# Performance work log

Measured on AMD Instinct MI355X. Metric: run time of the kernel, lower is better.

The kernel has to match this reference:

```python
import jax, jax.numpy as jnp
import numpy as np

ALPHA = 0.2  # LeakyReLU negative slope
NEG_INF = -9e15


def setup_inputs() -> dict:
    key = jax.random.key(0)
    k1, k2, k3, k4 = jax.random.split(key, 4)
    B, N, F_in, F_out = 8, 2048, 512, 256
    h = jax.random.normal(k1, (B, N, F_in), dtype=jnp.float32)
    adj = jax.random.randint(k2, (B, N, N), 0, 2, dtype=jnp.int32)
    W = jax.random.normal(k3, (F_in, F_out), dtype=jnp.float32) * (1.414 / np.sqrt(F_in))
    a = jax.random.normal(k4, (2 * F_out, 1), dtype=jnp.float32) * (1.414 / np.sqrt(2 * F_out))
    return {"h": h, "adj": adj, "W": W, "a": a}


def reference(h, adj, W, a):
    # Wh: [B, N, F_out]
    Wh = jnp.matmul(h, W)
    F_out = W.shape[1]
    a1 = a[:F_out, 0]   # [F_out] -> source (row i) part
    a2 = a[F_out:, 0]   # [F_out] -> target (col j) part
    # e[b,i,j] = leakyrelu(Wh[b,i]@a1 + Wh[b,j]@a2)  (decomposed concat-attention)
    f1 = jnp.einsum('bnf,f->bn', Wh, a1)  # [B, N]
    f2 = jnp.einsum('bnf,f->bn', Wh, a2)  # [B, N]
    e = f1[:, :, None] + f2[:, None, :]   # [B, N, N]
    e = jnp.where(e > 0, e, ALPHA * e)    # LeakyReLU
    e = jnp.where(adj > 0, e, NEG_INF)
    attention = jax.nn.softmax(e, axis=2)
    # dropout p=0.0 / eval mode: identity
    h_prime = jnp.matmul(attention, Wh)   # [B, N, F_out]
    return jax.nn.elu(h_prime)            # concat=True branch
```

## Files before the change

kernel.cpp:

```cpp
#include <hip/hip_runtime.h>
#include <hip/hip_bf16.h>

#define GAT_ALPHA 0.2f

typedef short bf16x8 __attribute__((ext_vector_type(8)));
typedef float f32x4 __attribute__((ext_vector_type(4)));

__device__ __forceinline__ unsigned f2bf_u(float x) {
  union { float f; unsigned u; } v; v.f = x;
  return (v.u + 0x7fffu + ((v.u >> 16) & 1u)) >> 16;
}
__device__ __forceinline__ unsigned short f2bf(float x) { return (unsigned short)f2bf_u(x); }

__global__ void k_wt(const float* __restrict__ W, unsigned short* __restrict__ WT) {
  int kb = blockIdx.x * 8;
  int f = threadIdx.x;
  bf16x8 o;
#pragma unroll
  for (int i = 0; i < 8; ++i) o[i] = (short)f2bf(W[(kb + i) * 256 + f]);
  *reinterpret_cast<bf16x8*>(WT + f * 512 + kb) = o;
}

__global__ __launch_bounds__(256, 2) void k_gemm1(
    const float* __restrict__ h, const unsigned short* __restrict__ WT,
    const float* __restrict__ avec,
    unsigned short* __restrict__ WhT,
    float* __restrict__ E1p, float* __restrict__ E1n,
    float* __restrict__ E2p, float* __restrict__ E2n)
{
  const int bx = blockIdx.x;
  const int b = bx & 7, ng = bx >> 3;
  const int n0 = ng * 32;
  const int t = threadIdx.x;
  const int lane = t & 63, w = t >> 6;
  const int l15 = lane & 15, q = lane >> 4;

  __shared__ __align__(16) unsigned short Wt[256 * 36];
  __shared__ float f1a[32], f2a[32];
  if (t < 32) { f1a[t] = 0.f; f2a[t] = 0.f; }

  f32x4 acc[4][2];
#pragma unroll
  for (int i = 0; i < 4; ++i)
#pragma unroll
    for (int j = 0; j < 2; ++j) acc[i][j] = (f32x4){0.f, 0.f, 0.f, 0.f};

  const size_t hbase = ((size_t)(b * 2048 + n0)) * 512;
  const unsigned short* wtb = WT + (w * 64 + l15) * 512 + q * 8;
  const float* hrow0 = h + hbase + (size_t)l15 * 512 + q * 8;
  const float* hrow1 = h + hbase + (size_t)(16 + l15) * 512 + q * 8;

  bf16x8 afA[4], afN[4];
  float4 hA[4], hB[4], hN[4];
#pragma unroll
  for (int mt = 0; mt < 4; ++mt) afA[mt] = *reinterpret_cast<const bf16x8*>(wtb + mt * 16 * 512);
  hA[0] = *reinterpret_cast<const float4*>(hrow0);
  hA[1] = *reinterpret_cast<const float4*>(hrow0 + 4);
  hA[2] = *reinterpret_cast<const float4*>(hrow1);
  hA[3] = *reinterpret_cast<const float4*>(hrow1 + 4);
  hB[0] = *reinterpret_cast<const float4*>(hrow0 + 32);
  hB[1] = *reinterpret_cast<const float4*>(hrow0 + 36);
  hB[2] = *reinterpret_cast<const float4*>(hrow1 + 32);
  hB[3] = *reinterpret_cast<const float4*>(hrow1 + 36);

#pragma unroll
  for (int k = 0; k < 16; ++k) {
    if (k < 15) {
      const unsigned short* p = wtb + (k + 1) * 32;
#pragma unroll
      for (int mt = 0; mt < 4; ++mt) afN[mt] = *reinterpret_cast<const bf16x8*>(p + mt * 16 * 512);
    }
    if (k < 14) {
      int o = (k + 2) * 32;
      hN[0] = *reinterpret_cast<const float4*>(hrow0 + o);
      hN[1] = *reinterpret_cast<const float4*>(hrow0 + o + 4);
      hN[2] = *reinterpret_cast<const float4*>(hrow1 + o);
      hN[3] = *reinterpret_cast<const float4*>(hrow1 + o + 4);
    }
    bf16x8 bfr[2];
#pragma unroll
    for (int nt = 0; nt < 2; ++nt) {
      float4 x0 = hA[nt * 2], x1 = hA[nt * 2 + 1];
      bf16x8 bb;
      bb[0] = (short)f2bf(x0.x); bb[1] = (short)f2bf(x0.y);
      bb[2] = (short)f2bf(x0.z); bb[3] = (short)f2bf(x0.w);
      bb[4] = (short)f2bf(x1.x); bb[5] = (short)f2bf(x1.y);
      bb[6] = (short)f2bf(x1.z); bb[7] = (short)f2bf(x1.w);
      bfr[nt] = bb;
    }
#pragma unroll
    for (int mt = 0; mt < 4; ++mt)
#pragma unroll
      for (int nt = 0; nt < 2; ++nt)
        acc[mt][nt] = __builtin_amdgcn_mfma_f32_16x16x32_bf16(afA[mt], bfr[nt], acc[mt][nt], 0, 0, 0);
    if (k < 15) {
#pragma unroll
      for (int mt = 0; mt < 4; ++mt) afA[mt] = afN[mt];
#pragma unroll
      for (int i = 0; i < 4; ++i) hA[i] = hB[i];
#pragma unroll
      for (int i = 0; i < 4; ++i) hB[i] = hN[i];
    }
  }

  float s1[2] = {0.f, 0.f}, s2[2] = {0.f, 0.f};
#pragma unroll
  for (int mt = 0; mt < 4; ++mt) {
#pragma unroll
    for (int nt = 0; nt < 2; ++nt) {
#pragma unroll
      for (int r = 0; r < 4; ++r) {
        int f = w * 64 + mt * 16 + q * 4 + r;
        float v = acc[mt][nt][r];
        Wt[f * 36 + nt * 16 + l15] = f2bf(v);
        s1[nt] += v * avec[f];
        s2[nt] += v * avec[256 + f];
      }
    }
  }
#pragma unroll
  for (int nt = 0; nt < 2; ++nt) {
    s1[nt] += __shfl_xor(s1[nt], 16); s1[nt] += __shfl_xor(s1[nt], 32);
    s2[nt] += __shfl_xor(s2[nt], 16); s2[nt] += __shfl_xor(s2[nt], 32);
  }
  __syncthreads();
  if (q == 0) {
#pragma unroll
    for (int nt = 0; nt < 2; ++nt) {
      atomicAdd(&f1a[nt * 16 + l15], s1[nt]);
      atomicAdd(&f2a[nt * 16 + l15], s2[nt]);
    }
  }
#pragma unroll
  for (int i = 0; i < 8; ++i) {
    int f = i * 32 + (t >> 3), g = t & 7;
    uint2 v = *reinterpret_cast<const uint2*>(Wt + f * 36 + g * 4);
    *reinterpret_cast<uint2*>(WhT + (size_t)(b * 256 + f) * 2048 + n0 + g * 4) = v;
  }
  __syncthreads();
  if (t < 32) {
    int n = b * 2048 + n0 + t;
    float f1 = f1a[t], f2 = f2a[t];
    E1p[n] = __expf(f1);
    E1n[n] = __expf(GAT_ALPHA * f1);
    E2p[n] = __expf(f2);
    E2n[n] = __expf(GAT_ALPHA * f2);
  }
}

__device__ __forceinline__ void build_frag(
    unsigned short* dst, int4 alo, int4 ahi, float e1p, float e1n,
    float4 epl, float4 eph, float4 enl, float4 enh, float& den)
{
  float p0 = alo.x ? fmaxf(e1p * epl.x, e1n * enl.x) : 0.f;
  float p1 = alo.y ? fmaxf(e1p * epl.y, e1n * enl.y) : 0.f;
  float p2 = alo.z ? fmaxf(e1p * epl.z, e1n * enl.z) : 0.f;
  float p3 = alo.w ? fmaxf(e1p * epl.w, e1n * enl.w) : 0.f;
  float p4 = ahi.x ? fmaxf(e1p * eph.x, e1n * enh.x) : 0.f;
  float p5 = ahi.y ? fmaxf(e1p * eph.y, e1n * enh.y) : 0.f;
  float p6 = ahi.z ? fmaxf(e1p * eph.z, e1n * enh.z) : 0.f;
  float p7 = ahi.w ? fmaxf(e1p * eph.w, e1n * enh.w) : 0.f;
  den += ((p0 + p1) + (p2 + p3)) + ((p4 + p5) + (p6 + p7));
  uint4 pk;
  pk.x = f2bf_u(p0) | (f2bf_u(p1) << 16);
  pk.y = f2bf_u(p2) | (f2bf_u(p3) << 16);
  pk.z = f2bf_u(p4) | (f2bf_u(p5) << 16);
  pk.w = f2bf_u(p6) | (f2bf_u(p7) << 16);
  *reinterpret_cast<uint4*>(dst) = pk;
}

__global__ __launch_bounds__(512, 2) void k_gat(
    const int* __restrict__ adj, const unsigned short* __restrict__ WhT,
    const float* __restrict__ E1p, const float* __restrict__ E1n,
    const float* __restrict__ E2p, const float* __restrict__ E2n,
    float* __restrict__ out)
{
  const int bx = blockIdx.x;
  const int b = bx & 7, ig = bx >> 3;
  const int i0 = ig * 64;
  const int t = threadIdx.x;
  const int lane = t & 63, w = t >> 6;
  const int l15 = lane & 15, q = lane >> 4;
  const int m = t & 15, qk = (t >> 4) & 3, pp = t >> 6;
  const int rt0 = pp >> 2, ks = pp & 3;
  const int r0 = rt0 * 16 + m, r1 = r0 + 32;
  const int cb = ks * 32 + qk * 8;

  __shared__ __align__(16) unsigned short Pb[2][8192];
  __shared__ float den_l[64];
  if (t < 64) den_l[t] = 0.f;

  const float e1p0 = E1p[b * 2048 + i0 + r0], e1n0 = E1n[b * 2048 + i0 + r0];
  const float e1p1 = E1p[b * 2048 + i0 + r1], e1n1 = E1n[b * 2048 + i0 + r1];
  float d0 = 0.f, d1 = 0.f;

  f32x4 acc[4][2];
#pragma unroll
  for (int i = 0; i < 4; ++i)
#pragma unroll
    for (int j = 0; j < 2; ++j) acc[i][j] = (f32x4){0.f, 0.f, 0.f, 0.f};

  const size_t adj0 = ((size_t)(b * 2048 + i0 + r0)) * 2048 + cb;
  const size_t adj1 = adj0 + (size_t)32 * 2048;
  const int e2b = b * 2048 + cb;
  const unsigned short* Wb = WhT + (size_t)(b * 256 + w * 32) * 2048;

  int4 z0l = *reinterpret_cast<const int4*>(adj + adj0);
  int4 z0h = *reinterpret_cast<const int4*>(adj + adj0 + 4);
  int4 z1l = *reinterpret_cast<const int4*>(adj + adj1);
  int4 z1h = *reinterpret_cast<const int4*>(adj + adj1 + 4);
  float4 zpl = *reinterpret_cast<const float4*>(E2p + e2b);
  float4 zph = *reinterpret_cast<const float4*>(E2p + e2b + 4);
  float4 znl = *reinterpret_cast<const float4*>(E2n + e2b);
  float4 znh = *reinterpret_cast<const float4*>(E2n + e2b + 4);
  bf16x8 bcur[2][4], bnxt[2][4];
#pragma unroll
  for (int ct = 0; ct < 2; ++ct)
#pragma unroll
    for (int k2 = 0; k2 < 4; ++k2)
      bcur[ct][k2] = *reinterpret_cast<const bf16x8*>(
          Wb + (size_t)(ct * 16 + l15) * 2048 + k2 * 32 + q * 8);
  int4 A0l = *reinterpret_cast<const int4*>(adj + adj0 + 128);
  int4 A0h = *reinterpret_cast<const int4*>(adj + adj0 + 132);
  int4 A1l = *reinterpret_cast<const int4*>(adj + adj1 + 128);
  int4 A1h = *reinterpret_cast<const int4*>(adj + adj1 + 132);
  float4 Epl = *reinterpret_cast<const float4*>(E2p + e2b + 128);
  float4 Eph = *reinterpret_cast<const float4*>(E2p + e2b + 132);
  float4 Enl = *reinterpret_cast<const float4*>(E2n + e2b + 128);
  float4 Enh = *reinterpret_cast<const float4*>(E2n + e2b + 132);
  build_frag(&Pb[0][(pp * 64 + lane) * 8], z0l, z0h, e1p0, e1n0, zpl, zph, znl, znh, d0);
  build_frag(&Pb[0][((pp + 8) * 64 + lane) * 8], z1l, z1h, e1p1, e1n1, zpl, zph, znl, znh, d1);
  __syncthreads();

#pragma unroll
  for (int c = 0; c < 16; ++c) {
    if (c < 15) {
      const unsigned short* p = Wb + (c + 1) * 128 + q * 8;
#pragma unroll
      for (int ct = 0; ct < 2; ++ct)
#pragma unroll
        for (int k2 = 0; k2 < 4; ++k2)
          bnxt[ct][k2] = *reinterpret_cast<const bf16x8*>(p + (size_t)(ct * 16 + l15) * 2048 + k2 * 32);
    }
    int4 nA0l, nA0h, nA1l, nA1h;
    float4 nEpl, nEph, nEnl, nEnh;
    if (c < 14) {
      int o = (c + 2) * 128;
      nA0l = *reinterpret_cast<const int4*>(adj + adj0 + o);
      nA0h = *reinterpret_cast<const int4*>(adj + adj0 + o + 4);
      nA1l = *reinterpret_cast<const int4*>(adj + adj1 + o);
      nA1h = *reinterpret_cast<const int4*>(adj + adj1 + o + 4);
      nEpl = *reinterpret_cast<const float4*>(E2p + e2b + o);
      nEph = *reinterpret_cast<const float4*>(E2p + e2b + o + 4);
      nEnl = *reinterpret_cast<const float4*>(E2n + e2b + o);
      nEnh = *reinterpret_cast<const float4*>(E2n + e2b + o + 4);
    }
    const unsigned short* pb = &Pb[c & 1][0];
#pragma unroll
    for (int k2 = 0; k2 < 4; ++k2) {
      bf16x8 afr[4];
#pragma unroll
      for (int rt = 0; rt < 4; ++rt)
        afr[rt] = *reinterpret_cast<const bf16x8*>(pb + ((rt * 4 + k2) * 64 + lane) * 8);
#pragma unroll
      for (int rt = 0; rt < 4; ++rt)
#pragma unroll
        for (int ct = 0; ct < 2; ++ct)
          acc[rt][ct] = __builtin_amdgcn_mfma_f32_16x16x32_bf16(afr[rt], bcur[ct][k2], acc[rt][ct], 0, 0, 0);
    }
    if (c < 15) {
      unsigned short* wb = &Pb[(c + 1) & 1][0];
      build_frag(wb + (pp * 64 + lane) * 8, A0l, A0h, e1p0, e1n0, Epl, Eph, Enl, Enh, d0);
      build_frag(wb + ((pp + 8) * 64 + lane) * 8, A1l, A1h, e1p1, e1n1, Epl, Eph, Enl, Enh, d1);
    }
    if (c < 15) __syncthreads();
    if (c < 15) {
#pragma unroll
      for (int ct = 0; ct < 2; ++ct)
#pragma unroll
        for (int k2 = 0; k2 < 4; ++k2) bcur[ct][k2] = bnxt[ct][k2];
    }
    if (c < 14) {
      A0l = nA0l; A0h = nA0h; A1l = nA1l; A1h = nA1h;
      Epl = nEpl; Eph = nEph; Enl = nEnl; Enh = nEnh;
    }
  }

  d0 += __shfl_xor(d0, 16); d0 += __shfl_xor(d0, 32);
  d1 += __shfl_xor(d1, 16); d1 += __shfl_xor(d1, 32);
  if (lane < 16) {
    atomicAdd(&den_l[r0], d0);
    atomicAdd(&den_l[r1], d1);
  }
  __syncthreads();

#pragma unroll
  for (int rt = 0; rt < 4; ++rt) {
#pragma unroll
    for (int r = 0; r < 4; ++r) {
      int row = rt * 16 + q * 4 + r;
      float dinv = 1.0f / den_l[row];
      size_t ob = ((size_t)(b * 2048 + i0 + row)) * 256 + w * 32;
#pragma unroll
      for (int ct = 0; ct < 2; ++ct) {
        float v = acc[rt][ct][r] * dinv;
        v = v > 0.f ? v : (__expf(v) - 1.f);
        out[ob + ct * 16 + l15] = v;
      }
    }
  }
}

extern "C" void kernel_launch(void* const* d_in, const int* in_sizes, int n_in,
                              void* d_out, int out_size, void* d_ws, size_t ws_size,
                              hipStream_t stream) {
  const float* h   = (const float*)d_in[0];
  const int*   adj = (const int*)d_in[1];
  const float* W   = (const float*)d_in[2];
  const float* a   = (const float*)d_in[3];
  float* out = (float*)d_out;

  char* ws = (char*)d_ws;
  unsigned short* WhT = (unsigned short*)ws;
  unsigned short* WT  = (unsigned short*)(ws + 8388608);
  float* E1p  = (float*)(ws + 8388608 + 262144);
  float* E1n  = E1p + 16384;
  float* E2p  = E1n + 16384;
  float* E2n  = E2p + 16384;

  k_wt<<<dim3(64), dim3(256), 0, stream>>>(W, WT);
  k_gemm1<<<dim3(512), dim3(256), 0, stream>>>(h, WT, a, WhT, E1p, E1n, E2p, E2n);
  k_gat<<<dim3(256), dim3(512), 0, stream>>>(adj, WhT, E1p, E1n, E2p, E2n, out);
}
```

Before: 262.3 us.

## Pack adjacency into bitmask, shrink gemm1 tile, simplify GAT pipelining

Adds a pre-pass kernel that packs the int32 adjacency into one bit per entry, in a layout matching the GAT fragment builder. The attention kernel then reads bytes instead of int4 vectors. k_gemm1 moves to 16-row tiles with a three-deep h prefetch and occupancy hint 4, and k_gat drops the register double-buffering of WhT and adj for in-loop loads with occupancy hint 4. The pack kernel still reads the full adjacency once and adds a launch, so the main gain must come from lighter register pressure and more occupancy, while lost prefetching may expose latency.

```diff
diff --git a/kernel.cpp b/kernel.cpp
--- a/kernel.cpp
+++ b/kernel.cpp
@@ -21,7 +21,26 @@
   *reinterpret_cast<bf16x8*>(WT + f * 512 + kb) = o;
 }
 
-__global__ __launch_bounds__(256, 2) void k_gemm1(
+__global__ __launch_bounds__(256) void k_pack(const int* __restrict__ adj,
+                                              unsigned char* __restrict__ bm) {
+  __shared__ unsigned char sb[2048];
+  const int bId = blockIdx.x, t = threadIdx.x;
+  const int4* base = reinterpret_cast<const int4*>(adj + (size_t)bId * 8 * 2048);
+#pragma unroll
+  for (int i = 0; i < 8; ++i) {
+    int4 v0 = base[i * 512 + t * 2];
+    int4 v1 = base[i * 512 + t * 2 + 1];
+    unsigned by = (v0.x != 0)        | ((v0.y != 0) << 1) | ((v0.z != 0) << 2) |
+                  ((v0.w != 0) << 3) | ((v1.x != 0) << 4) | ((v1.y != 0) << 5) |
+                  ((v1.z != 0) << 6) | ((v1.w != 0) << 7);
+    sb[i * 256 + (t & 15) * 16 + (t >> 4)] = (unsigned char)by;
+  }
+  __syncthreads();
+  reinterpret_cast<uint2*>(bm + (size_t)bId * 2048)[t] =
+      reinterpret_cast<const uint2*>(sb)[t];
+}
+
+__global__ __launch_bounds__(256, 4) void k_gemm1(
     const float* __restrict__ h, const unsigned short* __restrict__ WT,
     const float* __restrict__ avec,
     unsigned short* __restrict__ WhT,
@@ -30,115 +49,85 @@
 {
   const int bx = blockIdx.x;
   const int b = bx & 7, ng = bx >> 3;
-  const int n0 = ng * 32;
+  const int n0 = ng * 16;
   const int t = threadIdx.x;
   const int lane = t & 63, w = t >> 6;
   const int l15 = lane & 15, q = lane >> 4;
 
-  __shared__ __align__(16) unsigned short Wt[256 * 36];
-  __shared__ float f1a[32], f2a[32];
-  if (t < 32) { f1a[t] = 0.f; f2a[t] = 0.f; }
-
-  f32x4 acc[4][2];
-#pragma unroll
-  for (int i = 0; i < 4; ++i)
-#pragma unroll
-    for (int j = 0; j < 2; ++j) acc[i][j] = (f32x4){0.f, 0.f, 0.f, 0.f};
-
-  const size_t hbase = ((size_t)(b * 2048 + n0)) * 512;
+  __shared__ __align__(16) unsigned short Wt[256 * 24];
+  __shared__ float f1a[16], f2a[16];
+  if (t < 16) { f1a[t] = 0.f; f2a[t] = 0.f; }
+
+  f32x4 acc[4];
+#pragma unroll
+  for (int i = 0; i < 4; ++i) acc[i] = (f32x4){0.f, 0.f, 0.f, 0.f};
+
   const unsigned short* wtb = WT + (w * 64 + l15) * 512 + q * 8;
-  const float* hrow0 = h + hbase + (size_t)l15 * 512 + q * 8;
-  const float* hrow1 = h + hbase + (size_t)(16 + l15) * 512 + q * 8;
-
-  bf16x8 afA[4], afN[4];
-  float4 hA[4], hB[4], hN[4];
-#pragma unroll
-  for (int mt = 0; mt < 4; ++mt) afA[mt] = *reinterpret_cast<const bf16x8*>(wtb + mt * 16 * 512);
-  hA[0] = *reinterpret_cast<const float4*>(hrow0);
-  hA[1] = *reinterpret_cast<const float4*>(hrow0 + 4);
-  hA[2] = *reinterpret_cast<const float4*>(hrow1);
-  hA[3] = *reinterpret_cast<const float4*>(hrow1 + 4);
-  hB[0] = *reinterpret_cast<const float4*>(hrow0 + 32);
-  hB[1] = *reinterpret_cast<const float4*>(hrow0 + 36);
-  hB[2] = *reinterpret_cast<const float4*>(hrow1 + 32);
-  hB[3] = *reinterpret_cast<const float4*>(hrow1 + 36);
+  const float* hrow = h + ((size_t)(b * 2048 + n0 + l15)) * 512 + q * 8;
+
+  float4 hS0[2], hS1[2], hS2[2];
+  hS0[0] = *reinterpret_cast<const float4*>(hrow);
+  hS0[1] = *reinterpret_cast<const float4*>(hrow + 4);
+  hS1[0] = *reinterpret_cast<const float4*>(hrow + 32);
+  hS1[1] = *reinterpret_cast<const float4*>(hrow + 36);
+  hS2[0] = *reinterpret_cast<const float4*>(hrow + 64);
+  hS2[1] = *reinterpret_cast<const float4*>(hrow + 68);
 
 #pragma unroll
   for (int k = 0; k < 16; ++k) {
-    if (k < 15) {
-      const unsigned short* p = wtb + (k + 1) * 32;
-#pragma unroll
-      for (int mt = 0; mt < 4; ++mt) afN[mt] = *reinterpret_cast<const bf16x8*>(p + mt * 16 * 512);
-    }
-    if (k < 14) {
-      int o = (k + 2) * 32;
-      hN[0] = *reinterpret_cast<const float4*>(hrow0 + o);
-      hN[1] = *reinterpret_cast<const float4*>(hrow0 + o + 4);
-      hN[2] = *reinterpret_cast<const float4*>(hrow1 + o);
-      hN[3] = *reinterpret_cast<const float4*>(hrow1 + o + 4);
-    }
-    bf16x8 bfr[2];
-#pragma unroll
-    for (int nt = 0; nt < 2; ++nt) {
-      float4 x0 = hA[nt * 2], x1 = hA[nt * 2 + 1];
-      bf16x8 bb;
+    bf16x8 af[4];
+#pragma unroll
+    for (int mt = 0; mt < 4; ++mt)
+      af[mt] = *reinterpret_cast<const bf16x8*>(wtb + mt * 16 * 512 + k * 32);
+    float4 hN[2];
+    if (k < 13) {
+      hN[0] = *reinterpret_cast<const float4*>(hrow + (k + 3) * 32);
+      hN[1] = *reinterpret_cast<const float4*>(hrow + (k + 3) * 32 + 4);
+    }
+    bf16x8 bb;
+    {
+      float4 x0 = hS0[0], x1 = hS0[1];
       bb[0] = (short)f2bf(x0.x); bb[1] = (short)f2bf(x0.y);
       bb[2] = (short)f2bf(x0.z); bb[3] = (short)f2bf(x0.w);
       bb[4] = (short)f2bf(x1.x); bb[5] = (short)f2bf(x1.y);
       bb[6] = (short)f2bf(x1.z); bb[7] = (short)f2bf(x1.w);
-      bfr[nt] = bb;
     }
 #pragma unroll
     for (int mt = 0; mt < 4; ++mt)
-#pragma unroll
-      for (int nt = 0; nt < 2; ++nt)
-        acc[mt][nt] = __builtin_amdgcn_mfma_f32_16x16x32_bf16(afA[mt], bfr[nt], acc[mt][nt], 0, 0, 0);
-    if (k < 15) {
-#pragma unroll
-      for (int mt = 0; mt < 4; ++mt) afA[mt] = afN[mt];
-#pragma unroll
-      for (int i = 0; i < 4; ++i) hA[i] = hB[i];
-#pragma unroll
-      for (int i = 0; i < 4; ++i) hB[i] = hN[i];
-    }
-  }
-
-  float s1[2] = {0.f, 0.f}, s2[2] = {0.f, 0.f};
+      acc[mt] = __builtin_amdgcn_mfma_f32_16x16x32_bf16(af[mt], bb, acc[mt], 0, 0, 0);
+    hS0[0] = hS1[0]; hS0[1] = hS1[1];
+    hS1[0] = hS2[0]; hS1[1] = hS2[1];
+    if (k < 13) { hS2[0] = hN[0]; hS2[1] = hN[1]; }
+  }
+
+  float s1 = 0.f, s2 = 0.f;
 #pragma unroll
   for (int mt = 0; mt < 4; ++mt) {
 #pragma unroll
-    for (int nt = 0; nt < 2; ++nt) {
-#pragma unroll
-      for (int r = 0; r < 4; ++r) {
-        int f = w * 64 + mt * 16 + q * 4 + r;
-        float v = acc[mt][nt][r];
-        Wt[f * 36 + nt * 16 + l15] = f2bf(v);
-        s1[nt] += v * avec[f];
-        s2[nt] += v * avec[256 + f];
-      }
-    }
-  }
-#pragma unroll
-  for (int nt = 0; nt < 2; ++nt) {
-    s1[nt] += __shfl_xor(s1[nt], 16); s1[nt] += __shfl_xor(s1[nt], 32);
-    s2[nt] += __shfl_xor(s2[nt], 16); s2[nt] += __shfl_xor(s2[nt], 32);
-  }
+    for (int r = 0; r < 4; ++r) {
+      int f = w * 64 + mt * 16 + q * 4 + r;
+      float v = acc[mt][r];
+      Wt[f * 24 + l15] = f2bf(v);
+      s1 += v * avec[f];
+      s2 += v * avec[256 + f];
+    }
+  }
+  s1 += __shfl_xor(s1, 16); s1 += __shfl_xor(s1, 32);
+  s2 += __shfl_xor(s2, 16); s2 += __shfl_xor(s2, 32);
   __syncthreads();
   if (q == 0) {
-#pragma unroll
-    for (int nt = 0; nt < 2; ++nt) {
-      atomicAdd(&f1a[nt * 16 + l15], s1[nt]);
-      atomicAdd(&f2a[nt * 16 + l15], s2[nt]);
-    }
-  }
-#pragma unroll
-  for (int i = 0; i < 8; ++i) {
-    int f = i * 32 + (t >> 3), g = t & 7;
-    uint2 v = *reinterpret_cast<const uint2*>(Wt + f * 36 + g * 4);
-    *reinterpret_cast<uint2*>(WhT + (size_t)(b * 256 + f) * 2048 + n0 + g * 4) = v;
-  }
-  __syncthreads();
-  if (t < 32) {
+    atomicAdd(&f1a[l15], s1);
+    atomicAdd(&f2a[l15], s2);
+  }
+  {
+    uint4 va = *reinterpret_cast<const uint4*>(Wt + t * 24);
+    uint4 vb = *reinterpret_cast<const uint4*>(Wt + t * 24 + 8);
+    unsigned short* dst = WhT + (size_t)(b * 256 + t) * 2048 + n0;
+    *reinterpret_cast<uint4*>(dst) = va;
+    *reinterpret_cast<uint4*>(dst + 8) = vb;
+  }
+  __syncthreads();
+  if (t < 16) {
     int n = b * 2048 + n0 + t;
     float f1 = f1a[t], f2 = f2a[t];
     E1p[n] = __expf(f1);
@@ -149,17 +138,17 @@
 }
 
 __device__ __forceinline__ void build_frag(
-    unsigned short* dst, int4 alo, int4 ahi, float e1p, float e1n,
+    unsigned short* dst, unsigned by, float e1p, float e1n,
     float4 epl, float4 eph, float4 enl, float4 enh, float& den)
 {
-  float p0 = alo.x ? fmaxf(e1p * epl.x, e1n * enl.x) : 0.f;
-  float p1 = alo.y ? fmaxf(e1p * epl.y, e1n * enl.y) : 0.f;
-  float p2 = alo.z ? fmaxf(e1p * epl.z, e1n * enl.z) : 0.f;
-  float p3 = alo.w ? fmaxf(e1p * epl.w, e1n * enl.w) : 0.f;
-  float p4 = ahi.x ? fmaxf(e1p * eph.x, e1n * enh.x) : 0.f;
-  float p5 = ahi.y ? fmaxf(e1p * eph.y, e1n * enh.y) : 0.f;
-  float p6 = ahi.z ? fmaxf(e1p * eph.z, e1n * enh.z) : 0.f;
-  float p7 = ahi.w ? fmaxf(e1p * eph.w, e1n * enh.w) : 0.f;
+  float p0 = (by & 1u)   ? fmaxf(e1p * epl.x, e1n * enl.x) : 0.f;
+  float p1 = (by & 2u)   ? fmaxf(e1p * epl.y, e1n * enl.y) : 0.f;
+  float p2 = (by & 4u)   ? fmaxf(e1p * epl.z, e1n * enl.z) : 0.f;
+  float p3 = (by & 8u)   ? fmaxf(e1p * epl.w, e1n * enl.w) : 0.f;
+  float p4 = (by & 16u)  ? fmaxf(e1p * eph.x, e1n * enh.x) : 0.f;
+  float p5 = (by & 32u)  ? fmaxf(e1p * eph.y, e1n * enh.y) : 0.f;
+  float p6 = (by & 64u)  ? fmaxf(e1p * eph.z, e1n * enh.z) : 0.f;
+  float p7 = (by & 128u) ? fmaxf(e1p * eph.w, e1n * enh.w) : 0.f;
   den += ((p0 + p1) + (p2 + p3)) + ((p4 + p5) + (p6 + p7));
   uint4 pk;
   pk.x = f2bf_u(p0) | (f2bf_u(p1) << 16);
@@ -169,8 +158,8 @@
   *reinterpret_cast<uint4*>(dst) = pk;
 }
 
-__global__ __launch_bounds__(512, 2) void k_gat(
-    const int* __restrict__ adj, const unsigned short* __restrict__ WhT,
+__global__ __launch_bounds__(512, 4) void k_gat(
+    const unsigned char* __restrict__ bm, const unsigned short* __restrict__ WhT,
     const float* __restrict__ E1p, const float* __restrict__ E1n,
     const float* __restrict__ E2p, const float* __restrict__ E2n,
     float* __restrict__ out)
@@ -185,6 +174,7 @@
   const int rt0 = pp >> 2, ks = pp & 3;
   const int r0 = rt0 * 16 + m, r1 = r0 + 32;
   const int cb = ks * 32 + qk * 8;
+  const int K = ks * 4 + qk;
 
   __shared__ __align__(16) unsigned short Pb[2][8192];
   __shared__ float den_l[64];
@@ -200,56 +190,37 @@
 #pragma unroll
     for (int j = 0; j < 2; ++j) acc[i][j] = (f32x4){0.f, 0.f, 0.f, 0.f};
 
-  const size_t adj0 = ((size_t)(b * 2048 + i0 + r0)) * 2048 + cb;
-  const size_t adj1 = adj0 + (size_t)32 * 2048;
+  const unsigned char* bm0 = bm + ((size_t)(b * 2048 + i0 + r0)) * 256 + K * 16;
+  const unsigned char* bm1 = bm0 + (size_t)32 * 256;
   const int e2b = b * 2048 + cb;
   const unsigned short* Wb = WhT + (size_t)(b * 256 + w * 32) * 2048;
 
-  int4 z0l = *reinterpret_cast<const int4*>(adj + adj0);
-  int4 z0h = *reinterpret_cast<const int4*>(adj + adj0 + 4);
-  int4 z1l = *reinterpret_cast<const int4*>(adj + adj1);
-  int4 z1h = *reinterpret_cast<const int4*>(adj + adj1 + 4);
-  float4 zpl = *reinterpret_cast<const float4*>(E2p + e2b);
-  float4 zph = *reinterpret_cast<const float4*>(E2p + e2b + 4);
-  float4 znl = *reinterpret_cast<const float4*>(E2n + e2b);
-  float4 znh = *reinterpret_cast<const float4*>(E2n + e2b + 4);
-  bf16x8 bcur[2][4], bnxt[2][4];
-#pragma unroll
-  for (int ct = 0; ct < 2; ++ct)
-#pragma unroll
-    for (int k2 = 0; k2 < 4; ++k2)
-      bcur[ct][k2] = *reinterpret_cast<const bf16x8*>(
-          Wb + (size_t)(ct * 16 + l15) * 2048 + k2 * 32 + q * 8);
-  int4 A0l = *reinterpret_cast<const int4*>(adj + adj0 + 128);
-  int4 A0h = *reinterpret_cast<const int4*>(adj + adj0 + 132);
-  int4 A1l = *reinterpret_cast<const int4*>(adj + adj1 + 128);
-  int4 A1h = *reinterpret_cast<const int4*>(adj + adj1 + 132);
-  float4 Epl = *reinterpret_cast<const float4*>(E2p + e2b + 128);
-  float4 Eph = *reinterpret_cast<const float4*>(E2p + e2b + 132);
-  float4 Enl = *reinterpret_cast<const float4*>(E2n + e2b + 128);
-  float4 Enh = *reinterpret_cast<const float4*>(E2n + e2b + 132);
-  build_frag(&Pb[0][(pp * 64 + lane) * 8], z0l, z0h, e1p0, e1n0, zpl, zph, znl, znh, d0);
-  build_frag(&Pb[0][((pp + 8) * 64 + lane) * 8], z1l, z1h, e1p1, e1n1, zpl, zph, znl, znh, d1);
-  __syncthreads();
-
-#pragma unroll
+  {
+    unsigned by0 = bm0[0], by1 = bm1[0];
+    float4 epl = *reinterpret_cast<const float4*>(E2p + e2b);
+    float4 eph = *reinterpret_cast<const float4*>(E2p + e2b + 4);
+    float4 enl = *reinterpret_cast<const float4*>(E2n + e2b);
+    float4 enh = *reinterpret_cast<const float4*>(E2n + e2b + 4);
+    build_frag(&Pb[0][(pp * 64 + lane) * 8], by0, e1p0, e1n0, epl, eph, enl, enh, d0);
+    build_frag(&Pb[0][((pp + 8) * 64 + lane) * 8], by1, e1p1, e1n1, epl, eph, enl, enh, d1);
+  }
+  __syncthreads();
+
+#pragma unroll 2
   for (int c = 0; c < 16; ++c) {
+    bf16x8 bcur[2][4];
+#pragma unroll
+    for (int ct = 0; ct < 2; ++ct)
+#pragma unroll
+      for (int k2 = 0; k2 < 4; ++k2)
+        bcur[ct][k2] = *reinterpret_cast<const bf16x8*>(
+            Wb + (size_t)(ct * 16 + l15) * 2048 + c * 128 + k2 * 32 + q * 8);
+    unsigned nby0 = 0, nby1 = 0;
+    float4 nEpl, nEph, nEnl, nEnh;
     if (c < 15) {
-      const unsigned short* p = Wb + (c + 1) * 128 + q * 8;
-#pragma unroll
-      for (int ct = 0; ct < 2; ++ct)
-#pragma unroll
-        for (int k2 = 0; k2 < 4; ++k2)
-          bnxt[ct][k2] = *reinterpret_cast<const bf16x8*>(p + (size_t)(ct * 16 + l15) * 2048 + k2 * 32);
-    }
-    int4 nA0l, nA0h, nA1l, nA1h;
-    float4 nEpl, nEph, nEnl, nEnh;
-    if (c < 14) {
-      int o = (c + 2) * 128;
-      nA0l = *reinterpret_cast<const int4*>(adj + adj0 + o);
-      nA0h = *reinterpret_cast<const int4*>(adj + adj0 + o + 4);
-      nA1l = *reinterpret_cast<const int4*>(adj + adj1 + o);
-      nA1h = *reinterpret_cast<const int4*>(adj + adj1 + o + 4);
+      nby0 = bm0[c + 1];
+      nby1 = bm1[c + 1];
+      int o = (c + 1) * 128;
       nEpl = *reinterpret_cast<const float4*>(E2p + e2b + o);
       nEph = *reinterpret_cast<const float4*>(E2p + e2b + o + 4);
       nEnl = *reinterpret_cast<const float4*>(E2n + e2b + o);
@@ -270,19 +241,9 @@
     }
     if (c < 15) {
       unsigned short* wb = &Pb[(c + 1) & 1][0];
-      build_frag(wb + (pp * 64 + lane) * 8, A0l, A0h, e1p0, e1n0, Epl, Eph, Enl, Enh, d0);
-      build_frag(wb + ((pp + 8) * 64 + lane) * 8, A1l, A1h, e1p1, e1n1, Epl, Eph, Enl, Enh, d1);
-    }
-    if (c < 15) __syncthreads();
-    if (c < 15) {
-#pragma unroll
-      for (int ct = 0; ct < 2; ++ct)
-#pragma unroll
-        for (int k2 = 0; k2 < 4; ++k2) bcur[ct][k2] = bnxt[ct][k2];
-    }
-    if (c < 14) {
-      A0l = nA0l; A0h = nA0h; A1l = nA1l; A1h = nA1h;
-      Epl = nEpl; Eph = nEph; Enl = nEnl; Enh = nEnh;
+      build_frag(wb + (pp * 64 + lane) * 8, nby0, e1p0, e1n0, nEpl, nEph, nEnl, nEnh, d0);
+      build_frag(wb + ((pp + 8) * 64 + lane) * 8, nby1, e1p1, e1n1, nEpl, nEph, nEnl, nEnh, d1);
+      __syncthreads();
     }
   }
 
@@ -323,12 +284,14 @@
   char* ws = (char*)d_ws;
   unsigned short* WhT = (unsigned short*)ws;
   unsigned short* WT  = (unsigned short*)(ws + 8388608);
-  float* E1p  = (float*)(ws + 8388608 + 262144);
-  float* E1n  = E1p + 16384;
-  float* E2p  = E1n + 16384;
-  float* E2n  = E2p + 16384;
+  float* E1p = (float*)(ws + 8388608 + 262144);
+  float* E1n = E1p + 16384;
+  float* E2p = E1n + 16384;
+  float* E2n = E2p + 16384;
+  unsigned char* bm = (unsigned char*)(ws + 8388608 + 262144 + 4 * 65536);
 
   k_wt<<<dim3(64), dim3(256), 0, stream>>>(W, WT);
-  k_gemm1<<<dim3(512), dim3(256), 0, stream>>>(h, WT, a, WhT, E1p, E1n, E2p, E2n);
-  k_gat<<<dim3(256), dim3(512), 0, stream>>>(adj, WhT, E1p, E1n, E2p, E2n, out);
-}
+  k_pack<<<dim3(2048), dim3(256), 0, stream>>>(adj, bm);
+  k_gemm1<<<dim3(1024), dim3(256), 0, stream>>>(h, WT, a, WhT, E1p, E1n, E2p, E2n);
+  k_gat<<<dim3(256), dim3(512), 0, stream>>>(bm, WhT, E1p, E1n, E2p, E2n, out);
+}
```

Result: slower. 315.6 us (+20.3%).
